# Kernel optimization log

Hardware: AMD Instinct MI355X
Metric: run time of the kernel (lower is better)

The kernel has to match this reference:

```python
import jax, jax.numpy as jnp
import numpy as np

B, QT, KT = 4, 1024, 1024
Q_SIZE, K_SIZE, EMB, HEADS = 1024, 1024, 1024, 8
HEAD_DIM = EMB // HEADS


def setup_inputs() -> dict:
    key = jax.random.key(0)
    ks = jax.random.split(key, 8)
    query = jax.random.normal(ks[0], (B, QT, Q_SIZE), dtype=jnp.float32)
    key_t = jax.random.normal(ks[1], (B, KT, K_SIZE), dtype=jnp.float32)
    mask = jax.random.randint(ks[2], (B, QT, KT), 0, 2, dtype=jnp.int32)
    # Linear weights stored as (in, out); torch Linear computes x @ W.T, equivalent here.
    sq = 1.0 / np.sqrt(Q_SIZE)
    sk = 1.0 / np.sqrt(K_SIZE)
    se = 1.0 / np.sqrt(EMB)
    Wq = jax.random.uniform(ks[3], (Q_SIZE, EMB), jnp.float32, -sq, sq)
    Wk = jax.random.uniform(ks[4], (K_SIZE, EMB), jnp.float32, -sk, sk)
    Wv = jax.random.uniform(ks[5], (K_SIZE, EMB), jnp.float32, -sk, sk)
    Wu = jax.random.uniform(ks[6], (EMB, EMB), jnp.float32, -se, se)
    bu = jax.random.uniform(ks[7], (EMB,), jnp.float32, -se, se)
    return {"query": query, "key": key_t, "mask": mask,
            "Wq": Wq, "Wk": Wk, "Wv": Wv, "Wu": Wu, "bu": bu}


def reference(query, key, mask, Wq, Wk, Wv, Wu, bu):
    b, q_t, _ = query.shape
    k_t = key.shape[1]
    q = (query @ Wq).reshape(b, q_t, HEADS, HEAD_DIM)   # b i n d
    k = (key @ Wk).reshape(b, k_t, HEADS, HEAD_DIM)     # b j n d
    v = (key @ Wv).reshape(b, k_t, HEADS, HEAD_DIM)
    # NOTE: original module defines self.scale but never applies it.
    att_score = jnp.einsum('bind,bjnd->bijn', q, k)
    att_score = jnp.where(mask[..., None] == 0, jnp.float32(-1e9), att_score)
    att_prob = jax.nn.softmax(att_score, axis=2)        # softmax over key axis j
    att_vec = jnp.einsum('bijn,bjnd->bind', att_prob, v).reshape(b, q_t, EMB)
    return att_vec @ Wu + bu
```

## Files before the change

### kernel.cpp

```cpp
#include <hip/hip_runtime.h>
#include <hip/hip_bf16.h>


typedef __attribute__((ext_vector_type(8))) short bf16x8;
typedef __attribute__((ext_vector_type(4))) float f32x4;

static constexpr int BB = 4;
static constexpr int TT = 1024;
static constexpr int EE = 1024;
static constexpr int HH = 8;
static constexpr int DD = 128;

static __device__ __forceinline__ unsigned short f2b(float x) {
  union { float f; unsigned int u; } c; c.f = x;
  unsigned int r = c.u + 0x7fffu + ((c.u >> 16) & 1u);
  return (unsigned short)(r >> 16);
}

static __device__ __forceinline__ unsigned int cvtpk(float lo, float hi) {
  unsigned int r;
  asm("v_cvt_pk_bf16_f32 %0, %1, %2" : "=v"(r) : "v"(lo), "v"(hi));
  return r;
}

static __device__ __forceinline__ float exp2x(float x) {
  float r;
  asm("v_exp_f32 %0, %1" : "=v"(r) : "v"(x));
  return r;
}

static __device__ __forceinline__ unsigned opq(unsigned x) {
  unsigned y;
  asm("v_mov_b32 %0, %1" : "=v"(y) : "v"(x));
  return y;
}
static __device__ __forceinline__ float qred_max(float x) {
  unsigned a = __float_as_uint(x), b = opq(a);
  asm("v_permlane16_swap_b32 %0, %1" : "+v"(a), "+v"(b));
  float m = fmaxf(__uint_as_float(a), __uint_as_float(b));
  unsigned c = __float_as_uint(m), d = opq(c);
  asm("v_permlane32_swap_b32 %0, %1" : "+v"(c), "+v"(d));
  return fmaxf(__uint_as_float(c), __uint_as_float(d));
}
static __device__ __forceinline__ float qred_sum(float x) {
  unsigned a = __float_as_uint(x), b = opq(a);
  asm("v_permlane16_swap_b32 %0, %1" : "+v"(a), "+v"(b));
  float s = __uint_as_float(a) + __uint_as_float(b);
  unsigned c = __float_as_uint(s), d = opq(c);
  asm("v_permlane32_swap_b32 %0, %1" : "+v"(c), "+v"(d));
  return __uint_as_float(c) + __uint_as_float(d);
}
static __device__ __forceinline__ unsigned lx16(unsigned v, int lane) {
  unsigned a = v, b = opq(v);
  asm("v_permlane16_swap_b32 %0, %1" : "+v"(a), "+v"(b));
  return (lane & 16) ? a : b;
}
static __device__ __forceinline__ unsigned lx32(unsigned v, int lane) {
  unsigned a = v, b = opq(v);
  asm("v_permlane32_swap_b32 %0, %1" : "+v"(a), "+v"(b));
  return (lane & 32) ? a : b;
}

static __device__ __forceinline__ void gload_lds16(const void* g, void* l) {
  __builtin_amdgcn_global_load_lds(
      (const __attribute__((address_space(1))) unsigned int*)g,
      (__attribute__((address_space(3))) unsigned int*)l, 16, 0, 0);
}

struct PrepArgs {
  const float* qf; const float* kf;
  unsigned short* qb; unsigned short* kb;
  const float* wsrc[4]; unsigned short* wdst[4]; float wscale[4];
};

__global__ __launch_bounds__(256) void prep_kernel(PrepArgs a) {
  __shared__ float tile[32][33];
  const int bid = blockIdx.x, tid = threadIdx.x;
  if (bid < 4096) {
    int i = bid * 256 + tid;
    float4 va = ((const float4*)a.qf)[i];
    ushort4 oa; oa.x = f2b(va.x); oa.y = f2b(va.y);
    oa.z = f2b(va.z); oa.w = f2b(va.w);
    ((ushort4*)a.qb)[i] = oa;
    float4 vb = ((const float4*)a.kf)[i];
    ushort4 ob; ob.x = f2b(vb.x); ob.y = f2b(vb.y);
    ob.z = f2b(vb.z); ob.w = f2b(vb.w);
    ((ushort4*)a.kb)[i] = ob;
  } else {
    int g = bid - 4096;
    int wz = g >> 10, rem = g & 1023;
    int n0 = (rem & 31) * 32, k0 = (rem >> 5) * 32;
    const float* src = a.wsrc[wz];
    unsigned short* dst = a.wdst[wz];
    const float sc = a.wscale[wz];
    int tx = tid & 31, ty = tid >> 5;
#pragma unroll
    for (int i = 0; i < 4; ++i)
      tile[ty + i * 8][tx] = src[(size_t)(k0 + ty + i * 8) * EE + n0 + tx];
    __syncthreads();
#pragma unroll
    for (int i = 0; i < 4; ++i)
      dst[(size_t)(n0 + ty + i * 8) * EE + k0 + tx] =
          f2b(tile[tx][ty + i * 8] * sc);
  }
}

__global__ __launch_bounds__(256) void vtrans_mask_kernel(
    const unsigned short* __restrict__ vp, unsigned short* __restrict__ vt,
    const int* __restrict__ mask, unsigned long long* __restrict__ mbits) {
  __shared__ unsigned short tile[32][33];
  const int bid = blockIdx.x, tid = threadIdx.x;
  if (bid < 4096) {
    int x = bid & 3, y = (bid >> 2) & 31, z = bid >> 7;
    int b = z >> 3, h = z & 7;
    int d0 = x * 32, kt0 = y * 32;
    int tx = tid & 31, ty = tid >> 5;
#pragma unroll
    for (int i = 0; i < 4; ++i)
      tile[ty + i * 8][tx] =
          vp[(size_t)(b * TT + kt0 + ty + i * 8) * EE + h * DD + d0 + tx];
    __syncthreads();
#pragma unroll
    for (int i = 0; i < 4; ++i)
      vt[(size_t)((b * HH + h) * DD + d0 + ty + i * 8) * TT + kt0 + tx] =
          tile[tx][ty + i * 8];
  } else {
    int row = (bid - 4096) * 4 + (tid >> 6);
    int lane = tid & 63;
    const int* mrow = mask + (size_t)row * TT;
    unsigned long long myw = 0;
#pragma unroll
    for (int jw = 0; jw < 16; ++jw) {
      unsigned long long bal = __ballot(mrow[jw * 64 + lane] != 0);
      if (lane == jw) myw = bal;
    }
    if (lane < 16) mbits[(size_t)row * 16 + lane] = myw;
  }
}

static __device__ __forceinline__ void gemm_core(
    const unsigned short* __restrict__ A, const unsigned short* __restrict__ Bt,
    unsigned short* __restrict__ Cb, int bm, int bn) {
  constexpr int K = EE, N = EE;
  __shared__ __align__(16) unsigned short As[128 * 64];
  __shared__ __align__(16) unsigned short Bs[128 * 64];
  const int tid = threadIdx.x, lane = tid & 63, w = tid >> 6;
  const int wm = w >> 1, wn = w & 1;
  const int g4 = lane >> 4, l15 = lane & 15;

  f32x4 acc[4][4] = {};

  for (int kt = 0; kt < K / 64; ++kt) {
    const int k0 = kt * 64;
#pragma unroll
    for (int it = 0; it < 4; ++it) {
      int idx = it * 256 + tid;
      int r = idx >> 3, c = (idx & 7) ^ (r & 7);
      gload_lds16(A + (size_t)(bm * 128 + r) * K + k0 + c * 8, As + idx * 8);
      gload_lds16(Bt + (size_t)(bn * 128 + r) * K + k0 + c * 8, Bs + idx * 8);
    }
    __syncthreads();
    bf16x8 af[2][4], bf[2][4];
#pragma unroll
    for (int kc2 = 0; kc2 < 2; ++kc2) {
      int co = ((kc2 * 4 + g4) ^ (l15 & 7)) * 8;
#pragma unroll
      for (int i = 0; i < 4; ++i) {
        af[kc2][i] = *(const bf16x8*)(As + (wm * 64 + i * 16 + l15) * 64 + co);
        bf[kc2][i] = *(const bf16x8*)(Bs + (wn * 64 + i * 16 + l15) * 64 + co);
      }
    }
#pragma unroll
    for (int kc2 = 0; kc2 < 2; ++kc2)
#pragma unroll
      for (int i = 0; i < 4; ++i)
#pragma unroll
        for (int j = 0; j < 4; ++j)
          acc[i][j] = __builtin_amdgcn_mfma_f32_16x16x32_bf16(
              af[kc2][i], bf[kc2][j], acc[i][j], 0, 0, 0);
    __syncthreads();
  }

  const int rr = g4 * 4;
#pragma unroll
  for (int i = 0; i < 4; ++i)
#pragma unroll
    for (int j = 0; j < 4; ++j) {
      int row = bm * 128 + wm * 64 + i * 16 + rr;
      int col = bn * 128 + wn * 64 + j * 16 + l15;
#pragma unroll
      for (int r = 0; r < 4; ++r)
        Cb[(size_t)(row + r) * N + col] = f2b(acc[i][j][r]);
    }
}

struct Gemm3 { const unsigned short* A[3]; const unsigned short* Bt[3];
               unsigned short* C[3]; };

__global__ __launch_bounds__(256) void proj_gemm_kernel(Gemm3 g) {
  const int orig = blockIdx.x + 32 * blockIdx.y + 256 * blockIdx.z;
  const int lin = (orig & 7) * 96 + (orig >> 3);
  const int z = lin >> 8, rem = lin & 255;
  const int bn = rem >> 5, bm = rem & 31;
  gemm_core(g.A[z], g.Bt[z], g.C[z], bm, bn);
}

__global__ __launch_bounds__(256) void out_gemm_kernel(
    const unsigned short* __restrict__ A, const unsigned short* __restrict__ Bt,
    float* __restrict__ Cf, const float* __restrict__ bias) {
  constexpr int K = EE, N = EE;
  __shared__ __align__(16) unsigned short As[64 * 64];
  __shared__ __align__(16) unsigned short Bs[128 * 64];
  const int tid = threadIdx.x, lane = tid & 63, w = tid >> 6;
  const int wm = w >> 1, wn = w & 1;
  const int orig = blockIdx.x + 64 * blockIdx.y;
  const int lin = (orig & 7) * 64 + (orig >> 3);
  const int bn = lin >> 6, bm = lin & 63;
  const int g4 = lane >> 4, l15 = lane & 15;

  f32x4 acc[2][4] = {};

  for (int kt = 0; kt < K / 64; ++kt) {
    const int k0 = kt * 64;
#pragma unroll
    for (int it = 0; it < 2; ++it) {
      int idx = it * 256 + tid;
      int r = idx >> 3, c = (idx & 7) ^ (r & 7);
      gload_lds16(A + (size_t)(bm * 64 + r) * K + k0 + c * 8, As + idx * 8);
    }
#pragma unroll
    for (int it = 0; it < 4; ++it) {
      int idx = it * 256 + tid;
      int r = idx >> 3, c = (idx & 7) ^ (r & 7);
      gload_lds16(Bt + (size_t)(bn * 128 + r) * K + k0 + c * 8, Bs + idx * 8);
    }
    __syncthreads();
    bf16x8 af[2][2], bf[2][4];
#pragma unroll
    for (int kc2 = 0; kc2 < 2; ++kc2) {
      int co = ((kc2 * 4 + g4) ^ (l15 & 7)) * 8;
#pragma unroll
      for (int i = 0; i < 2; ++i)
        af[kc2][i] = *(const bf16x8*)(As + (wm * 32 + i * 16 + l15) * 64 + co);
#pragma unroll
      for (int j = 0; j < 4; ++j)
        bf[kc2][j] = *(const bf16x8*)(Bs + (wn * 64 + j * 16 + l15) * 64 + co);
    }
#pragma unroll
    for (int kc2 = 0; kc2 < 2; ++kc2)
#pragma unroll
      for (int i = 0; i < 2; ++i)
#pragma unroll
        for (int j = 0; j < 4; ++j)
          acc[i][j] = __builtin_amdgcn_mfma_f32_16x16x32_bf16(
              af[kc2][i], bf[kc2][j], acc[i][j], 0, 0, 0);
    __syncthreads();
  }

  const int rr = g4 * 4;
#pragma unroll
  for (int i = 0; i < 2; ++i)
#pragma unroll
    for (int j = 0; j < 4; ++j) {
      int row = bm * 64 + wm * 32 + i * 16 + rr;
      int col = bn * 128 + wn * 64 + j * 16 + l15;
#pragma unroll
      for (int r = 0; r < 4; ++r)
        Cf[(size_t)(row + r) * N + col] = acc[i][j][r] + bias[col];
    }
}

__global__ __launch_bounds__(512, 4) void attn_kernel(
    const unsigned short* __restrict__ q, const unsigned short* __restrict__ k,
    const unsigned short* __restrict__ vt,
    const unsigned long long* __restrict__ mbits,
    unsigned short* __restrict__ av) {
  extern __shared__ __align__(16) char smem[];

  const int tid = threadIdx.x, lane = tid & 63, w = tid >> 6;
  const int grp = w >> 2, qw = w & 3;
  const int orig = blockIdx.x + 16 * blockIdx.y + 128 * blockIdx.z;
  const int qt = (orig >> 3) & 15;
  const int pair = ((orig & 7) << 2) | (orig >> 7);
  const int h = pair & 7, b = pair >> 3;
  const int i0 = qt * 64 + qw * 16;
  const int g4 = lane >> 4, l15 = lane & 15;
  const int swz = (l15 & 7) << 4;

  bf16x8 aq[4];
  {
    const unsigned short* qb =
        q + (size_t)(b * TT + i0 + l15) * EE + h * DD + g4 * 8;
#pragma unroll
    for (int kc = 0; kc < 4; ++kc) aq[kc] = *(const bf16x8*)(qb + kc * 32);
  }

  const unsigned short* sptr[4];
  int ldsb[4];
  size_t sadv;
  if (w < 4) {
    int kg = w >> 1, kh = w & 1;
    const unsigned short* kb0 = k + (size_t)(b * TT) * EE + h * DD;
#pragma unroll
    for (int p = 0; p < 4; ++p) {
      int idx = kh * 256 + p * 64 + lane;
      int kr = idx >> 4, c = (idx & 15) ^ (kr & 7);
      sptr[p] = kb0 + (size_t)(kg * 512 + kr) * EE + c * 8;
      ldsb[p] = kg * 8192 + (kh * 256 + p * 64) * 16;
    }
    sadv = (size_t)32 * EE;
  } else {
    int vw = w - 4;
    const unsigned short* vb0 = vt + (size_t)((b * HH + h) * DD) * TT;
#pragma unroll
    for (int p = 0; p < 4; ++p) {
      int cid = vw * 256 + p * 64 + lane;
      int d = cid >> 3, slot = cid & 7, eff = slot ^ (d & 7);
      sptr[p] = vb0 + (size_t)d * TT + (eff >> 2) * 512 + (eff & 3) * 8;
      ldsb[p] = 32768 + (vw * 256 + p * 64) * 16;
    }
    sadv = 32;
  }

  const unsigned* mb32 =
      (const unsigned*)mbits + ((size_t)(b * TT + i0 + l15) << 5) + grp * 16;
  unsigned mcur = mb32[0];

  int kb_[4];
#pragma unroll
  for (int kc = 0; kc < 4; ++kc)
    kb_[kc] = grp * 8192 + l15 * 256 + ((kc * 64 + g4 * 16) ^ swz);
  const int vb_ = 32768 + l15 * 128 + (((grp * 4 + g4) ^ (l15 & 7)) << 4);

#pragma unroll
  for (int p = 0; p < 4; ++p) gload_lds16(sptr[p], smem + ldsb[p]);
#pragma unroll
  for (int p = 0; p < 4; ++p) sptr[p] += sadv;

  f32x4 oacc[8] = {};
  float mrun = -__builtin_inff(), lrun = 0.f;

  __syncthreads();
  int bufoff = 0;

  for (int t = 0; t < 16; ++t) {
    unsigned mnext = 0;
    if (t < 15) {
      mnext = mb32[t + 1];
      int dst = bufoff ^ 16384;
#pragma unroll
      for (int p = 0; p < 4; ++p) gload_lds16(sptr[p], smem + dst + ldsb[p]);
#pragma unroll
      for (int p = 0; p < 4; ++p) sptr[p] += sadv;
    }

    f32x4 sacc[2] = {};
    __builtin_amdgcn_s_setprio(1);
#pragma unroll
    for (int kc = 0; kc < 4; ++kc)
#pragma unroll
      for (int nt = 0; nt < 2; ++nt) {
        bf16x8 bk = *(const bf16x8*)(smem + bufoff + kb_[kc] + nt * 4096);
        sacc[nt] = __builtin_amdgcn_mfma_f32_16x16x32_bf16(bk, aq[kc],
                                                           sacc[nt], 0, 0, 0);
      }
    __builtin_amdgcn_s_setprio(0);

#pragma unroll
    for (int nt = 0; nt < 2; ++nt)
#pragma unroll
      for (int r = 0; r < 4; ++r)
        if (((mcur >> (nt * 16 + g4 * 4 + r)) & 1u) == 0u)
          sacc[nt][r] = -1e9f;

    float mx = sacc[0][0];
#pragma unroll
    for (int nt = 0; nt < 2; ++nt)
#pragma unroll
      for (int r = 0; r < 4; ++r) mx = fmaxf(mx, sacc[nt][r]);
    mx = qred_max(mx);

    if (__any(mx > mrun + 8.f)) {
      float mnew = fmaxf(mrun, mx);
      float sc = exp2x(mrun - mnew);
      lrun *= sc;
      mrun = mnew;
      float scO[4];
#pragma unroll
      for (int r = 0; r < 4; ++r)
        scO[r] = __shfl(sc, (lane & 48) | (((lane & 48) >> 2) + r), 64);
#pragma unroll
      for (int dt = 0; dt < 8; ++dt)
#pragma unroll
        for (int r = 0; r < 4; ++r) oacc[dt][r] *= scO[r];
    }

    float p2[2][4];
    float s0 = 0.f;
#pragma unroll
    for (int nt = 0; nt < 2; ++nt)
#pragma unroll
      for (int r = 0; r < 4; ++r) {
        float pv = exp2x(sacc[nt][r] - mrun);
        p2[nt][r] = pv;
        s0 += pv;
      }
    lrun += qred_sum(s0);

    unsigned int paw[4];
    {
      unsigned int D0a = cvtpk(p2[0][0], p2[0][1]);
      unsigned int D1a = cvtpk(p2[0][2], p2[0][3]);
      unsigned int D0b = cvtpk(p2[1][0], p2[1][1]);
      unsigned int D1b = cvtpk(p2[1][2], p2[1][3]);
      unsigned int r1 = lx16(g4 < 2 ? D0a : D0b, lane);
      unsigned int r2 = lx16(g4 < 2 ? D1a : D1b, lane);
      unsigned int r3 = lx32(g4 == 0 ? D0b : D0a, lane);
      unsigned int r4 = lx32(g4 == 0 ? D1b : D1a, lane);
      unsigned int r5 = lx16(lx32(g4 == 2 ? D0a : D0b, lane), lane);
      unsigned int r6 = lx16(lx32(g4 == 2 ? D1a : D1b, lane), lane);
      paw[0] = g4 == 0 ? D0a : g4 == 1 ? r5 : g4 == 2 ? r3 : r1;
      paw[1] = g4 == 0 ? D1a : g4 == 1 ? r6 : g4 == 2 ? r4 : r2;
      paw[2] = g4 == 0 ? r1 : g4 == 1 ? r3 : g4 == 2 ? r5 : D0b;
      paw[3] = g4 == 0 ? r2 : g4 == 1 ? r4 : g4 == 2 ? r6 : D1b;
    }

    __builtin_amdgcn_s_setprio(1);
    {
      union { unsigned int u[4]; bf16x8 v; } pau;
      pau.u[0] = paw[0]; pau.u[1] = paw[1];
      pau.u[2] = paw[2]; pau.u[3] = paw[3];
#pragma unroll
      for (int dt = 0; dt < 8; ++dt) {
        bf16x8 bv = *(const bf16x8*)(smem + bufoff + vb_ + dt * 2048);
        oacc[dt] = __builtin_amdgcn_mfma_f32_16x16x32_bf16(pau.v, bv, oacc[dt],
                                                           0, 0, 0);
      }
    }
    __builtin_amdgcn_s_setprio(0);

    __syncthreads();
    bufoff ^= 16384;
    mcur = mnext;
  }

  if (grp == 1) {
    char* ob = smem + qw * 8192 + lane * 128;
#pragma unroll
    for (int dt = 0; dt < 8; ++dt)
      *(f32x4*)(ob + ((dt ^ (lane & 7)) * 16)) = oacc[dt];
    float* mlb = (float*)(smem + 32768 + qw * 512 + lane * 8);
    mlb[0] = mrun; mlb[1] = lrun;
  }
  __syncthreads();
  if (grp == 0) {
    const char* ob = smem + qw * 8192 + lane * 128;
    const float* mlb = (const float*)(smem + 32768 + qw * 512 + lane * 8);
    float m2 = mlb[0], l2 = mlb[1];
    float ms = fmaxf(mrun, m2);
    float a1 = exp2x(mrun - ms), a2 = exp2x(m2 - ms);
    float lt = lrun * a1 + l2 * a2;
    float a1O[4], a2O[4], linv[4];
#pragma unroll
    for (int r = 0; r < 4; ++r) {
      int src = (lane & 48) | (((lane & 48) >> 2) + r);
      a1O[r] = __shfl(a1, src, 64);
      a2O[r] = __shfl(a2, src, 64);
      linv[r] = 1.f / __shfl(lt, src, 64);
    }
    unsigned short* obp =
        av + (size_t)(b * TT + i0 + g4 * 4) * EE + h * DD + l15;
#pragma unroll
    for (int dt = 0; dt < 8; ++dt) {
      f32x4 o2 = *(const f32x4*)(ob + ((dt ^ (lane & 7)) * 16));
#pragma unroll
      for (int r = 0; r < 4; ++r)
        obp[(size_t)r * EE + dt * 16] =
            f2b((oacc[dt][r] * a1O[r] + o2[r] * a2O[r]) * linv[r]);
    }
  }
}

extern "C" void kernel_launch(void* const* d_in, const int* in_sizes, int n_in,
                              void* d_out, int out_size, void* d_ws,
                              size_t ws_size, hipStream_t stream) {
  const float* query = (const float*)d_in[0];
  const float* key   = (const float*)d_in[1];
  const int*   mask  = (const int*)d_in[2];
  const float* Wq    = (const float*)d_in[3];
  const float* Wk    = (const float*)d_in[4];
  const float* Wv    = (const float*)d_in[5];
  const float* Wu    = (const float*)d_in[6];
  const float* bu    = (const float*)d_in[7];
  float* out = (float*)d_out;

  char* ws = (char*)d_ws;
  const size_t MB = 1024 * 1024;
  unsigned short* qbf = (unsigned short*)(ws);
  unsigned short* kbf = (unsigned short*)(ws + 8 * MB);
  unsigned short* Wqt = (unsigned short*)(ws + 16 * MB);
  unsigned short* Wkt = (unsigned short*)(ws + 18 * MB);
  unsigned short* Wvt = (unsigned short*)(ws + 20 * MB);
  unsigned short* Wut = (unsigned short*)(ws + 22 * MB);
  unsigned short* qp  = (unsigned short*)(ws + 24 * MB);
  unsigned short* kp  = (unsigned short*)(ws + 32 * MB);
  unsigned short* vp  = (unsigned short*)(ws + 40 * MB);
  unsigned short* vtb = (unsigned short*)(ws + 48 * MB);
  unsigned short* av  = (unsigned short*)(ws + 56 * MB);
  unsigned long long* mbt = (unsigned long long*)(ws);

  PrepArgs pa;
  pa.qf = query; pa.kf = key; pa.qb = qbf; pa.kb = kbf;
  pa.wsrc[0] = Wq; pa.wsrc[1] = Wk; pa.wsrc[2] = Wv; pa.wsrc[3] = Wu;
  pa.wdst[0] = Wqt; pa.wdst[1] = Wkt; pa.wdst[2] = Wvt; pa.wdst[3] = Wut;
  pa.wscale[0] = 1.4426950408889634f;
  pa.wscale[1] = 1.0f; pa.wscale[2] = 1.0f; pa.wscale[3] = 1.0f;
  prep_kernel<<<8192, 256, 0, stream>>>(pa);

  Gemm3 g3;
  g3.A[0] = qbf; g3.A[1] = kbf; g3.A[2] = kbf;
  g3.Bt[0] = Wqt; g3.Bt[1] = Wkt; g3.Bt[2] = Wvt;
  g3.C[0] = qp; g3.C[1] = kp; g3.C[2] = vp;
  proj_gemm_kernel<<<dim3(32, 8, 3), 256, 0, stream>>>(g3);

  vtrans_mask_kernel<<<5120, 256, 0, stream>>>(vp, vtb, mask, mbt);

  attn_kernel<<<dim3(16, 8, 4), 512, 65536, stream>>>(qp, kp, vtb, mbt, av);

  out_gemm_kernel<<<dim3(64, 8), 256, 0, stream>>>(av, Wut, out, bu);
}
```

Before: 107.1 us.

## Fuse K and V projections into one GEMM sharing the A tile

The K and V projections both read the same key activations, so one block now loads the A tile once and multiplies it against both Wk and Wv, holding two accumulator sets. The Q projection runs in separate blocks with a single B operand. This cuts redundant A-tile global loads and the block count from 768 to 512. The cost is load imbalance between fused and unfused blocks, higher register pressure from the doubled accumulators, larger LDS use that may reduce occupancy, and removal of the previous L2-friendly block swizzle.

```diff
diff --git a/kernel.cpp b/kernel.cpp
--- a/kernel.cpp
+++ b/kernel.cpp
@@ -138,17 +138,30 @@
   }
 }
 
-static __device__ __forceinline__ void gemm_core(
-    const unsigned short* __restrict__ A, const unsigned short* __restrict__ Bt,
-    unsigned short* __restrict__ Cb, int bm, int bn) {
+struct GemmP {
+  const unsigned short* qA; const unsigned short* kA;
+  const unsigned short* WqT; const unsigned short* WkT; const unsigned short* WvT;
+  unsigned short* qC; unsigned short* kC; unsigned short* vC;
+};
+
+__global__ __launch_bounds__(256) void proj_gemm_kernel(GemmP g) {
   constexpr int K = EE, N = EE;
   __shared__ __align__(16) unsigned short As[128 * 64];
-  __shared__ __align__(16) unsigned short Bs[128 * 64];
+  __shared__ __align__(16) unsigned short Bs0[128 * 64];
+  __shared__ __align__(16) unsigned short Bs1[128 * 64];
   const int tid = threadIdx.x, lane = tid & 63, w = tid >> 6;
   const int wm = w >> 1, wn = w & 1;
+  const int bm = blockIdx.x, bn = blockIdx.y;
+  const bool fused = (blockIdx.z == 0);
+  const unsigned short* A  = fused ? g.kA : g.qA;
+  const unsigned short* B0 = fused ? g.WkT : g.WqT;
+  const unsigned short* B1 = g.WvT;
+  unsigned short* C0 = fused ? g.kC : g.qC;
+  unsigned short* C1 = g.vC;
   const int g4 = lane >> 4, l15 = lane & 15;
 
-  f32x4 acc[4][4] = {};
+  f32x4 acc0[4][4] = {};
+  f32x4 acc1[4][4] = {};
 
   for (int kt = 0; kt < K / 64; ++kt) {
     const int k0 = kt * 64;
@@ -156,28 +169,40 @@
     for (int it = 0; it < 4; ++it) {
       int idx = it * 256 + tid;
       int r = idx >> 3, c = (idx & 7) ^ (r & 7);
-      gload_lds16(A + (size_t)(bm * 128 + r) * K + k0 + c * 8, As + idx * 8);
-      gload_lds16(Bt + (size_t)(bn * 128 + r) * K + k0 + c * 8, Bs + idx * 8);
-    }
-    __syncthreads();
-    bf16x8 af[2][4], bf[2][4];
+      gload_lds16(A  + (size_t)(bm * 128 + r) * K + k0 + c * 8, As  + idx * 8);
+      gload_lds16(B0 + (size_t)(bn * 128 + r) * K + k0 + c * 8, Bs0 + idx * 8);
+      if (fused)
+        gload_lds16(B1 + (size_t)(bn * 128 + r) * K + k0 + c * 8, Bs1 + idx * 8);
+    }
+    __syncthreads();
 #pragma unroll
     for (int kc2 = 0; kc2 < 2; ++kc2) {
       int co = ((kc2 * 4 + g4) ^ (l15 & 7)) * 8;
+      bf16x8 af[4], b0[4];
 #pragma unroll
       for (int i = 0; i < 4; ++i) {
-        af[kc2][i] = *(const bf16x8*)(As + (wm * 64 + i * 16 + l15) * 64 + co);
-        bf[kc2][i] = *(const bf16x8*)(Bs + (wn * 64 + i * 16 + l15) * 64 + co);
+        af[i] = *(const bf16x8*)(As  + (wm * 64 + i * 16 + l15) * 64 + co);
+        b0[i] = *(const bf16x8*)(Bs0 + (wn * 64 + i * 16 + l15) * 64 + co);
       }
-    }
-#pragma unroll
-    for (int kc2 = 0; kc2 < 2; ++kc2)
 #pragma unroll
       for (int i = 0; i < 4; ++i)
 #pragma unroll
         for (int j = 0; j < 4; ++j)
-          acc[i][j] = __builtin_amdgcn_mfma_f32_16x16x32_bf16(
-              af[kc2][i], bf[kc2][j], acc[i][j], 0, 0, 0);
+          acc0[i][j] = __builtin_amdgcn_mfma_f32_16x16x32_bf16(
+              af[i], b0[j], acc0[i][j], 0, 0, 0);
+      if (fused) {
+        bf16x8 b1[4];
+#pragma unroll
+        for (int j = 0; j < 4; ++j)
+          b1[j] = *(const bf16x8*)(Bs1 + (wn * 64 + j * 16 + l15) * 64 + co);
+#pragma unroll
+        for (int i = 0; i < 4; ++i)
+#pragma unroll
+          for (int j = 0; j < 4; ++j)
+            acc1[i][j] = __builtin_amdgcn_mfma_f32_16x16x32_bf16(
+                af[i], b1[j], acc1[i][j], 0, 0, 0);
+      }
+    }
     __syncthreads();
   }
 
@@ -189,20 +214,12 @@
       int row = bm * 128 + wm * 64 + i * 16 + rr;
       int col = bn * 128 + wn * 64 + j * 16 + l15;
 #pragma unroll
-      for (int r = 0; r < 4; ++r)
-        Cb[(size_t)(row + r) * N + col] = f2b(acc[i][j][r]);
-    }
-}
-
-struct Gemm3 { const unsigned short* A[3]; const unsigned short* Bt[3];
-               unsigned short* C[3]; };
-
-__global__ __launch_bounds__(256) void proj_gemm_kernel(Gemm3 g) {
-  const int orig = blockIdx.x + 32 * blockIdx.y + 256 * blockIdx.z;
-  const int lin = (orig & 7) * 96 + (orig >> 3);
-  const int z = lin >> 8, rem = lin & 255;
-  const int bn = rem >> 5, bm = rem & 31;
-  gemm_core(g.A[z], g.Bt[z], g.C[z], bm, bn);
+      for (int r = 0; r < 4; ++r) {
+        C0[(size_t)(row + r) * N + col] = f2b(acc0[i][j][r]);
+        if (fused)
+          C1[(size_t)(row + r) * N + col] = f2b(acc1[i][j][r]);
+      }
+    }
 }
 
 __global__ __launch_bounds__(256) void out_gemm_kernel(
@@ -517,11 +534,11 @@
   pa.wscale[1] = 1.0f; pa.wscale[2] = 1.0f; pa.wscale[3] = 1.0f;
   prep_kernel<<<8192, 256, 0, stream>>>(pa);
 
-  Gemm3 g3;
-  g3.A[0] = qbf; g3.A[1] = kbf; g3.A[2] = kbf;
-  g3.Bt[0] = Wqt; g3.Bt[1] = Wkt; g3.Bt[2] = Wvt;
-  g3.C[0] = qp; g3.C[1] = kp; g3.C[2] = vp;
-  proj_gemm_kernel<<<dim3(32, 8, 3), 256, 0, stream>>>(g3);
+  GemmP gp;
+  gp.qA = qbf; gp.kA = kbf;
+  gp.WqT = Wqt; gp.WkT = Wkt; gp.WvT = Wvt;
+  gp.qC = qp; gp.kC = kp; gp.vC = vp;
+  proj_gemm_kernel<<<dim3(32, 8, 2), 256, 0, stream>>>(gp);
 
   vtrans_mask_kernel<<<5120, 256, 0, stream>>>(vp, vtb, mask, mbt);
 
```

After: 120.1 us. 1.12x slower.

## Fuse V transpose into projection GEMM epilogue via swizzled LDS staging

Applied to the files above, without the earlier changes.

The V projection GEMM blocks now write their output transposed directly into the per-head V^T layout. They stage the tile in LDS with an XOR swizzle and then issue 16-byte global stores. This removes the separate transpose pass and the write-then-read round trip of the intermediate vp buffer. The mask bit-packing becomes its own small kernel. In exchange, the V blocks' epilogue gains an LDS round trip and an extra barrier, and the gather reads 16 scalar shorts per thread.

```diff
diff --git a/kernel.cpp b/kernel.cpp
--- a/kernel.cpp
+++ b/kernel.cpp
@@ -105,47 +105,37 @@
   }
 }
 
-__global__ __launch_bounds__(256) void vtrans_mask_kernel(
-    const unsigned short* __restrict__ vp, unsigned short* __restrict__ vt,
+__global__ __launch_bounds__(256) void maskpack_kernel(
     const int* __restrict__ mask, unsigned long long* __restrict__ mbits) {
-  __shared__ unsigned short tile[32][33];
-  const int bid = blockIdx.x, tid = threadIdx.x;
-  if (bid < 4096) {
-    int x = bid & 3, y = (bid >> 2) & 31, z = bid >> 7;
-    int b = z >> 3, h = z & 7;
-    int d0 = x * 32, kt0 = y * 32;
-    int tx = tid & 31, ty = tid >> 5;
-#pragma unroll
-    for (int i = 0; i < 4; ++i)
-      tile[ty + i * 8][tx] =
-          vp[(size_t)(b * TT + kt0 + ty + i * 8) * EE + h * DD + d0 + tx];
-    __syncthreads();
-#pragma unroll
-    for (int i = 0; i < 4; ++i)
-      vt[(size_t)((b * HH + h) * DD + d0 + ty + i * 8) * TT + kt0 + tx] =
-          tile[tx][ty + i * 8];
-  } else {
-    int row = (bid - 4096) * 4 + (tid >> 6);
-    int lane = tid & 63;
-    const int* mrow = mask + (size_t)row * TT;
-    unsigned long long myw = 0;
-#pragma unroll
-    for (int jw = 0; jw < 16; ++jw) {
-      unsigned long long bal = __ballot(mrow[jw * 64 + lane] != 0);
-      if (lane == jw) myw = bal;
-    }
-    if (lane < 16) mbits[(size_t)row * 16 + lane] = myw;
-  }
-}
-
-static __device__ __forceinline__ void gemm_core(
-    const unsigned short* __restrict__ A, const unsigned short* __restrict__ Bt,
-    unsigned short* __restrict__ Cb, int bm, int bn) {
+  int row = blockIdx.x * 4 + (threadIdx.x >> 6);
+  int lane = threadIdx.x & 63;
+  const int* mrow = mask + (size_t)row * TT;
+  unsigned long long myw = 0;
+#pragma unroll
+  for (int jw = 0; jw < 16; ++jw) {
+    unsigned long long bal = __ballot(mrow[jw * 64 + lane] != 0);
+    if (lane == jw) myw = bal;
+  }
+  if (lane < 16) mbits[(size_t)row * 16 + lane] = myw;
+}
+
+struct Gemm3 { const unsigned short* A[3]; const unsigned short* Bt[3];
+               unsigned short* C[2]; };
+
+__global__ __launch_bounds__(256) void proj_gemm_kernel(
+    Gemm3 g, unsigned short* __restrict__ vtb) {
   constexpr int K = EE, N = EE;
-  __shared__ __align__(16) unsigned short As[128 * 64];
-  __shared__ __align__(16) unsigned short Bs[128 * 64];
+  __shared__ __align__(16) unsigned short sm[128 * 128];
+  unsigned short* As = sm;
+  unsigned short* Bs = sm + 128 * 64;
   const int tid = threadIdx.x, lane = tid & 63, w = tid >> 6;
   const int wm = w >> 1, wn = w & 1;
+  const int orig = blockIdx.x + 32 * blockIdx.y + 256 * blockIdx.z;
+  const int lin = (orig & 7) * 96 + (orig >> 3);
+  const int z = lin >> 8, rem = lin & 255;
+  const int bn = rem >> 5, bm = rem & 31;
+  const unsigned short* A = g.A[z];
+  const unsigned short* Bt = g.Bt[z];
   const int g4 = lane >> 4, l15 = lane & 15;
 
   f32x4 acc[4][4] = {};
@@ -182,27 +172,51 @@
   }
 
   const int rr = g4 * 4;
-#pragma unroll
-  for (int i = 0; i < 4; ++i)
-#pragma unroll
-    for (int j = 0; j < 4; ++j) {
-      int row = bm * 128 + wm * 64 + i * 16 + rr;
-      int col = bn * 128 + wn * 64 + j * 16 + l15;
-#pragma unroll
-      for (int r = 0; r < 4; ++r)
-        Cb[(size_t)(row + r) * N + col] = f2b(acc[i][j][r]);
-    }
-}
-
-struct Gemm3 { const unsigned short* A[3]; const unsigned short* Bt[3];
-               unsigned short* C[3]; };
-
-__global__ __launch_bounds__(256) void proj_gemm_kernel(Gemm3 g) {
-  const int orig = blockIdx.x + 32 * blockIdx.y + 256 * blockIdx.z;
-  const int lin = (orig & 7) * 96 + (orig >> 3);
-  const int z = lin >> 8, rem = lin & 255;
-  const int bn = rem >> 5, bm = rem & 31;
-  gemm_core(g.A[z], g.Bt[z], g.C[z], bm, bn);
+  if (z < 2) {
+    unsigned short* Cb = g.C[z];
+#pragma unroll
+    for (int i = 0; i < 4; ++i)
+#pragma unroll
+      for (int j = 0; j < 4; ++j) {
+        int row = bm * 128 + wm * 64 + i * 16 + rr;
+        int col = bn * 128 + wn * 64 + j * 16 + l15;
+#pragma unroll
+        for (int r = 0; r < 4; ++r)
+          Cb[(size_t)(row + r) * N + col] = f2b(acc[i][j][r]);
+      }
+  } else {
+#pragma unroll
+    for (int i = 0; i < 4; ++i)
+#pragma unroll
+      for (int j = 0; j < 4; ++j) {
+        int d = wn * 64 + j * 16 + l15;
+#pragma unroll
+        for (int r = 0; r < 4; ++r) {
+          int row = wm * 64 + i * 16 + rr + r;
+          int addr = d * 256 + ((((row >> 3) ^ (d & 7)) & 15) << 4)
+                   + (row & 7) * 2;
+          *(unsigned short*)((char*)sm + addr) = f2b(acc[i][j][r]);
+        }
+      }
+    __syncthreads();
+    const int b = bm >> 3, kt0 = (bm & 7) * 128;
+    unsigned short* vb = vtb + (size_t)((b * HH + bn) * DD) * TT + kt0;
+#pragma unroll
+    for (int p = 0; p < 4; ++p) {
+      int u = p * 256 + tid;
+      int d = u >> 3, kc = u & 7;
+      __align__(16) unsigned short tmp[16];
+#pragma unroll
+      for (int e = 0; e < 16; ++e) {
+        int row = kc * 16 + e;
+        int addr = d * 256 + ((((row >> 3) ^ (d & 7)) & 15) << 4)
+                 + (row & 7) * 2;
+        tmp[e] = *(const unsigned short*)((const char*)sm + addr);
+      }
+      *(uint4*)(vb + (size_t)d * TT + kc * 16)     = *(const uint4*)&tmp[0];
+      *(uint4*)(vb + (size_t)d * TT + kc * 16 + 8) = *(const uint4*)&tmp[8];
+    }
+  }
 }
 
 __global__ __launch_bounds__(256) void out_gemm_kernel(
@@ -504,7 +518,6 @@
   unsigned short* Wut = (unsigned short*)(ws + 22 * MB);
   unsigned short* qp  = (unsigned short*)(ws + 24 * MB);
   unsigned short* kp  = (unsigned short*)(ws + 32 * MB);
-  unsigned short* vp  = (unsigned short*)(ws + 40 * MB);
   unsigned short* vtb = (unsigned short*)(ws + 48 * MB);
   unsigned short* av  = (unsigned short*)(ws + 56 * MB);
   unsigned long long* mbt = (unsigned long long*)(ws);
@@ -520,10 +533,10 @@
   Gemm3 g3;
   g3.A[0] = qbf; g3.A[1] = kbf; g3.A[2] = kbf;
   g3.Bt[0] = Wqt; g3.Bt[1] = Wkt; g3.Bt[2] = Wvt;
-  g3.C[0] = qp; g3.C[1] = kp; g3.C[2] = vp;
-  proj_gemm_kernel<<<dim3(32, 8, 3), 256, 0, stream>>>(g3);
-
-  vtrans_mask_kernel<<<5120, 256, 0, stream>>>(vp, vtb, mask, mbt);
+  g3.C[0] = qp; g3.C[1] = kp;
+  proj_gemm_kernel<<<dim3(32, 8, 3), 256, 0, stream>>>(g3, vtb);
+
+  maskpack_kernel<<<1024, 256, 0, stream>>>(mask, mbt);
 
   attn_kernel<<<dim3(16, 8, 4), 512, 65536, stream>>>(qp, kp, vtb, mbt, av);
 
```

New measurement: 115.1 us. +7.5%, slower.
